# Kernel tuning notes

Hardware: AMD Instinct MI355X
Metric: run time of the kernel (lower is better)

The kernel has to match this reference:

```python
import jax, jax.numpy as jnp
import numpy as np
from jax import lax

# GlobalSeed with a standard Mamba2 (SSD) core.
# C=64 feature channels, G=8 token dim, d_inner=16, d_state=16, nheads=2, headdim=8, d_conv=3.
C_FEAT, G, D_INNER, D_STATE, NHEADS, HEADDIM, D_CONV = 64, 8, 16, 16, 2, 8, 3
CONV_DIM = D_INNER + 2 * D_STATE  # 48
D_IN_PROJ = 2 * D_INNER + 2 * D_STATE + NHEADS  # 66


def setup_inputs() -> dict:
    key = jax.random.key(0)
    ks = jax.random.split(key, 16)
    B, H, W = 16, 128, 128
    s = 0.02
    return {
        "x": jax.random.normal(ks[0], (B, C_FEAT, H, W), jnp.float32),
        "tok_w": s * jax.random.normal(ks[1], (G, C_FEAT), jnp.float32),
        "tok_b": jnp.zeros((G,), jnp.float32),
        "detok_w": s * jax.random.normal(ks[2], (C_FEAT, G), jnp.float32),
        "detok_b": jnp.zeros((C_FEAT,), jnp.float32),
        "in_proj_w": s * jax.random.normal(ks[3], (D_IN_PROJ, G), jnp.float32),
        "in_proj_b": jnp.zeros((D_IN_PROJ,), jnp.float32),
        "conv_w": s * jax.random.normal(ks[4], (CONV_DIM, D_CONV), jnp.float32),
        "conv_b": jnp.zeros((CONV_DIM,), jnp.float32),
        "A_log": jnp.log(jnp.arange(1, NHEADS + 1, dtype=jnp.float32)),
        "D": jnp.ones((NHEADS,), jnp.float32),
        "dt_bias": 0.1 * jax.random.normal(ks[5], (NHEADS,), jnp.float32),
        "norm_w": jnp.ones((D_INNER,), jnp.float32),
        "out_w": s * jax.random.normal(ks[6], (G, D_INNER), jnp.float32),
        "out_b": jnp.zeros((G,), jnp.float32),
    }


def _mamba2(gt, in_proj_w, in_proj_b, conv_w, conv_b, A_log, D, dt_bias, norm_w, out_w, out_b):
    # gt: (B, L, G) tokens
    B, L, _ = gt.shape
    zxbcdt = gt @ in_proj_w.T + in_proj_b  # (B, L, 66)
    z = zxbcdt[..., :D_INNER]
    xBC = zxbcdt[..., D_INNER:D_INNER + CONV_DIM]
    dt = zxbcdt[..., D_INNER + CONV_DIM:]  # (B, L, nheads)
    # depthwise causal conv1d over L
    xBC = lax.conv_general_dilated(
        xBC.transpose(0, 2, 1), conv_w[:, None, :], (1,), [(D_CONV - 1, 0)],
        feature_group_count=CONV_DIM).transpose(0, 2, 1) + conv_b
    xBC = jax.nn.silu(xBC)
    xr = xBC[..., :D_INNER].reshape(B, L, NHEADS, HEADDIM)
    Bm = xBC[..., D_INNER:D_INNER + D_STATE]   # (B, L, N)
    Cm = xBC[..., D_INNER + D_STATE:]          # (B, L, N)
    dt = jax.nn.softplus(dt + dt_bias)          # (B, L, H)
    dec = jnp.exp(dt * (-jnp.exp(A_log)))       # (B, L, H)

    def step(h, inp):
        xt, Bt, Ct, dtt, dct = inp  # (B,H,P) (B,N) (B,N) (B,H) (B,H)
        h = dct[:, :, None, None] * h + (dtt[:, :, None] * xt)[..., None] * Bt[:, None, None, :]
        y = jnp.einsum('bhpn,bn->bhp', h, Ct)
        return h, y

    h0 = jnp.zeros((B, NHEADS, HEADDIM, D_STATE), gt.dtype)
    xs = (xr.transpose(1, 0, 2, 3), Bm.transpose(1, 0, 2), Cm.transpose(1, 0, 2),
          dt.transpose(1, 0, 2), dec.transpose(1, 0, 2))
    _, ys = lax.scan(step, h0, xs)  # (L, B, H, P)
    y = ys.transpose(1, 0, 2, 3) + D[None, None, :, None] * xr
    y = y.reshape(B, L, D_INNER)
    y = y * jax.nn.silu(z)  # gated
    y = y * lax.rsqrt(jnp.mean(y * y, axis=-1, keepdims=True) + 1e-5) * norm_w  # RMSNormGated
    return y @ out_w.T + out_b  # (B, L, G)


def reference(x, tok_w, tok_b, detok_w, detok_b, in_proj_w, in_proj_b, conv_w, conv_b,
              A_log, D, dt_bias, norm_w, out_w, out_b):
    B, C, H, W = x.shape
    L = H * W
    g = jnp.einsum('bchw,gc->bghw', x, tok_w) + tok_b[None, :, None, None]
    gt = g.reshape(B, G, L).transpose(0, 2, 1)  # (B, L, G)
    gt = _mamba2(gt, in_proj_w, in_proj_b, conv_w, conv_b, A_log, D, dt_bias, norm_w, out_w, out_b) + gt
    g2 = gt.transpose(0, 2, 1).reshape(B, G, H, W)
    return x + jnp.einsum('bghw,cg->bchw', g2, detok_w) + detok_b[None, :, None, None]
```

## Files before the change

### kernel.cpp

```cpp
#include <hip/hip_runtime.h>
#include <math.h>

#define NB 16
#define CF 64
#define LL 16384
#define GG 8
#define NH 2
#define CHN 64
#define NCH 256
#define NGRP 16

static constexpr size_t OFF_GT = 0;
static constexpr size_t OFF_U2 = OFF_GT + (size_t)NB*LL*GG;
static constexpr size_t OFF_AC = OFF_U2 + (size_t)NB*NCH*256;
static constexpr size_t OFF_PH = OFF_AC + (size_t)NB*NCH*NH;
static constexpr size_t OFF_CP = OFF_PH + (size_t)NB*NCH*256;
static constexpr size_t OFF_UG = OFF_CP + (size_t)NB*NCH*NH;
static constexpr size_t OFF_AG = OFF_UG + (size_t)NB*NGRP*256;
static constexpr size_t OFF_GH = OFF_AG + (size_t)NB*NGRP*NH;
static constexpr size_t OFF_G2 = OFF_GH + (size_t)NB*NGRP*256;
static constexpr size_t OFF_ST = OFF_G2 + (size_t)NB*LL*GG;
static constexpr size_t WS_FLOATS = OFF_ST + (size_t)NB*NCH*1792;

typedef float f32x4 __attribute__((ext_vector_type(4)));
typedef short bf16x8 __attribute__((ext_vector_type(8)));

__device__ __forceinline__ float siluf(float v){ return v / (1.f + __expf(-v)); }
__device__ __forceinline__ float softplusf(float v){ return v > 20.f ? v : log1pf(__expf(v)); }

__device__ __forceinline__ unsigned short f2bf(float f){
    unsigned int u = __float_as_uint(f);
    u += 0x7fffu + ((u >> 16) & 1u);
    return (unsigned short)(u >> 16);
}
__device__ __forceinline__ float bf2f(unsigned short s){
    return __uint_as_float(((unsigned int)s) << 16);
}
__device__ __forceinline__ unsigned int pack2bf(float lo, float hi){
    return (unsigned int)f2bf(lo) | ((unsigned int)f2bf(hi) << 16);
}
__device__ __forceinline__ unsigned int packtr(float lo, float hi){
    return (__float_as_uint(hi) & 0xffff0000u) | (__float_as_uint(lo) >> 16);
}

__device__ __forceinline__ void load8(float* d, const float* p){
    float4 a = ((const float4*)p)[0];
    float4 b = ((const float4*)p)[1];
    d[0]=a.x; d[1]=a.y; d[2]=a.z; d[3]=a.w;
    d[4]=b.x; d[5]=b.y; d[6]=b.z; d[7]=b.w;
}

__global__ __launch_bounds__(64) void k1a_tok(
    const float* __restrict__ x, const float* __restrict__ tok_w,
    const float* __restrict__ tok_b, float* __restrict__ gtw)
{
    __shared__ float s_tok[GG*CF];
    int tid = threadIdx.x;
    int b  = blockIdx.x >> 6;
    int ck = blockIdx.x & 63;
    int l0 = (ck << 8) + (tid << 2);
    for (int i = tid; i < GG*CF; i += 64) s_tok[i] = tok_w[i];
    __syncthreads();
    float acc[4][GG];
    #pragma unroll
    for (int r = 0; r < 4; ++r)
        #pragma unroll
        for (int g = 0; g < GG; ++g) acc[r][g] = tok_b[g];
    const float* xb = x + (size_t)b*CF*LL + l0;
    #pragma unroll 8
    for (int c = 0; c < CF; ++c) {
        float4 xv = *(const float4*)(xb + (size_t)c*LL);
        float xa[4] = {xv.x, xv.y, xv.z, xv.w};
        #pragma unroll
        for (int g = 0; g < GG; ++g) {
            float w = s_tok[g*CF + c];
            #pragma unroll
            for (int r = 0; r < 4; ++r) acc[r][g] = fmaf(xa[r], w, acc[r][g]);
        }
    }
    float* gp = gtw + ((size_t)b*LL + l0)*GG;
    #pragma unroll
    for (int r = 0; r < 4; ++r) {
        ((float4*)gp)[r*2+0] = make_float4(acc[r][0],acc[r][1],acc[r][2],acc[r][3]);
        ((float4*)gp)[r*2+1] = make_float4(acc[r][4],acc[r][5],acc[r][6],acc[r][7]);
    }
}

__device__ __forceinline__ void build_W(
    int tid, const float* ipw, const float* ipb, const float* cw, const float* cb,
    unsigned short* Wt, float* s_bias, float* s_c0, float* s_c1, float* s_wdt)
{
    int col = tid & 63, kb = tid >> 6;
    unsigned int wd0=0u, wd1=0u, wd2=0u, wd3=0u;
    if (col < 48) {
        if (kb < 3) {
            float cwv = cw[col*3 + (2-kb)];
            const float* iprow = ipw + (16+col)*8;
            wd0 = pack2bf(iprow[0]*cwv, iprow[1]*cwv);
            wd1 = pack2bf(iprow[2]*cwv, iprow[3]*cwv);
            wd2 = pack2bf(iprow[4]*cwv, iprow[5]*cwv);
            wd3 = pack2bf(iprow[6]*cwv, iprow[7]*cwv);
        }
    } else if (kb == 0) {
        const float* iprow = ipw + (col-48)*8;
        wd0 = pack2bf(iprow[0], iprow[1]);
        wd1 = pack2bf(iprow[2], iprow[3]);
        wd2 = pack2bf(iprow[4], iprow[5]);
        wd3 = pack2bf(iprow[6], iprow[7]);
    }
    *(uint4*)&Wt[col*32 + kb*8] = make_uint4(wd0,wd1,wd2,wd3);
    if (kb == 0) {
        float bias;
        if (col < 48) {
            float w0 = cw[col*3], w1 = cw[col*3+1], w2 = cw[col*3+2];
            float ib = ipb[16+col];
            bias = cb[col] + ib*(w0+w1+w2);
            s_c0[col] = ib*(w0+w1);
            s_c1[col] = ib*w0;
        } else bias = ipb[col-48];
        s_bias[col] = bias;
    } else if (kb == 1 && col < 16) s_wdt[col] = ipw[512 + col];
}

__global__ __launch_bounds__(256) void k2a_state(
    const float* __restrict__ gtw,
    const float* __restrict__ ipw, const float* __restrict__ ipb,
    const float* __restrict__ cw, const float* __restrict__ cb,
    const float* __restrict__ A_log, const float* __restrict__ dt_bias,
    float* __restrict__ stw,
    float* __restrict__ U2w, float* __restrict__ Acw)
{
    __shared__ __align__(16) unsigned short Wt[64*32];
    __shared__ float s_bias[64], s_c0[48], s_c1[48], s_wdt[16];
    __shared__ __align__(16) unsigned short XTbf[16*72];
    __shared__ __align__(16) unsigned short BTbf[16*72];
    __shared__ __align__(16) unsigned short WXbf[16*72];
    __shared__ __align__(16) unsigned short Brow[64*16];
    __shared__ __align__(16) unsigned short Crow[64*16];
    __shared__ float s_dt[64][2], s_nda[64][2], s_w[64][2];

    int tid = threadIdx.x;
    int b = blockIdx.x >> 8, c = blockIdx.x & 255;
    float* stp = stw + ((size_t)(b*NCH + c))*1792;
    build_W(tid, ipw, ipb, cw, cb, Wt, s_bias, s_c0, s_c1, s_wdt);
    __syncthreads();

    float a0e = __expf(A_log[0]), a1e = __expf(A_log[1]);
    float dtb0 = dt_bias[0], dtb1 = dt_bias[1];
    float bdt0 = ipb[64], bdt1 = ipb[65];

    int lane = tid & 63, wv = tid >> 6;
    int ar = lane & 15, kb = lane >> 4;
    int trow = wv*16 + kb*4;

    float fr[8];
    bf16x8 aop = {0,0,0,0,0,0,0,0};
    int rowi = c*CHN + wv*16 + ar - kb;
    if (kb < 3 && rowi >= 0) {
        load8(fr, gtw + ((size_t)b*LL + rowi)*GG);
        unsigned int* ap = (unsigned int*)&aop;
        ap[0] = pack2bf(fr[0],fr[1]); ap[1] = pack2bf(fr[2],fr[3]);
        ap[2] = pack2bf(fr[4],fr[5]); ap[3] = pack2bf(fr[6],fr[7]);
    }
    f32x4 st0, st1, st2;
    {
        float b0 = s_bias[ar], b1 = s_bias[16+ar], b2 = s_bias[32+ar];
        f32x4 c0v = {b0,b0,b0,b0}, c1v = {b1,b1,b1,b1}, c2v = {b2,b2,b2,b2};
        st0 = __builtin_amdgcn_mfma_f32_16x16x32_bf16(aop, *(const bf16x8*)&Wt[ar*32 + kb*8],      c0v, 0,0,0);
        st1 = __builtin_amdgcn_mfma_f32_16x16x32_bf16(aop, *(const bf16x8*)&Wt[(16+ar)*32 + kb*8], c1v, 0,0,0);
        st2 = __builtin_amdgcn_mfma_f32_16x16x32_bf16(aop, *(const bf16x8*)&Wt[(32+ar)*32 + kb*8], c2v, 0,0,0);
    }
    if (c == 0 && wv == 0 && kb == 0) {
        st0[0] -= s_c0[ar];    st0[1] -= s_c1[ar];
        st1[0] -= s_c0[16+ar]; st1[1] -= s_c1[16+ar];
        st2[0] -= s_c0[32+ar]; st2[1] -= s_c1[32+ar];
    }
    if (kb == 0) {
        float d0 = bdt0, d1 = bdt1;
        #pragma unroll
        for (int g = 0; g < 8; ++g) {
            d0 = fmaf(fr[g], s_wdt[g],   d0);
            d1 = fmaf(fr[g], s_wdt[8+g], d1);
        }
        float dt0 = softplusf(d0 + dtb0), dt1 = softplusf(d1 + dtb1);
        int row = wv*16 + ar;
        s_dt[row][0] = dt0; s_dt[row][1] = dt1;
        s_nda[row][0] = -dt0*a0e; s_nda[row][1] = -dt1*a1e;
    }
    {
        float v0 = siluf(st0[0]), v1 = siluf(st0[1]), v2 = siluf(st0[2]), v3 = siluf(st0[3]);
        *(uint2*)&XTbf[ar*72 + trow] = make_uint2(pack2bf(v0,v1), pack2bf(v2,v3));
        float b0 = siluf(st1[0]), b1 = siluf(st1[1]), b2 = siluf(st1[2]), b3 = siluf(st1[3]);
        *(uint2*)&BTbf[ar*72 + trow] = make_uint2(pack2bf(b0,b1), pack2bf(b2,b3));
        float bb[4] = {b0,b1,b2,b3};
        #pragma unroll
        for (int rg = 0; rg < 4; ++rg) {
            float vB = bb[rg];
            float vC = siluf(st2[rg]);
            float pB = __shfl_xor(vB, 1);
            float pC = __shfl_xor(vC, 1);
            if (!(ar & 1)) {
                *(unsigned int*)&Brow[(trow+rg)*16 + ar] = pack2bf(vB, pB);
                *(unsigned int*)&Crow[(trow+rg)*16 + ar] = pack2bf(vC, pC);
            }
        }
    }
    __syncthreads();

    if (tid < 64) {
        int rr = tid;
        float v0 = s_nda[rr][0], v1 = s_nda[rr][1];
        #pragma unroll
        for (int off = 1; off < 64; off <<= 1) {
            float t0 = __shfl_up(v0, off);
            float t1 = __shfl_up(v1, off);
            if (rr >= off) { v0 += t0; v1 += t1; }
        }
        float f0 = __shfl(v0, 63), f1 = __shfl(v1, 63);
        s_w[rr][0] = __expf(f0 - v0) * s_dt[rr][0];
        s_w[rr][1] = __expf(f1 - v1) * s_dt[rr][1];
        stp[1536 + rr*2 + 0] = v0;
        stp[1536 + rr*2 + 1] = v1;
        stp[1664 + rr*2 + 0] = s_dt[rr][0];
        stp[1664 + rr*2 + 1] = s_dt[rr][1];
        if (rr == 63)
            *(float2*)(Acw + ((size_t)b*NCH + c)*2) = make_float2(__expf(f0), __expf(f1));
    }
    __syncthreads();

    {
        unsigned int* stX = (unsigned int*)stp;
        unsigned int* stB = (unsigned int*)(stp + 512);
        unsigned int* stC = (unsigned int*)(stp + 1024);
        if (tid < 128) {
            int p = tid >> 3, seg = tid & 7;
            int s0 = seg*8, he = p >> 3;
            const unsigned short* xp = &XTbf[p*72 + s0];
            unsigned int wd[4];
            #pragma unroll
            for (int j = 0; j < 4; ++j) {
                float lo = bf2f(xp[2*j])   * s_w[s0+2*j][he];
                float hi = bf2f(xp[2*j+1]) * s_w[s0+2*j+1][he];
                wd[j] = pack2bf(lo, hi);
            }
            *(uint4*)&WXbf[p*72 + s0] = make_uint4(wd[0],wd[1],wd[2],wd[3]);
            int row = tid >> 1, hf = tid & 1;
            *(uint4*)&stB[row*8 + hf*4] = *(const uint4*)&Brow[row*16 + hf*8];
        } else {
            int i = tid - 128;
            int p = i >> 3, seg = i & 7;
            *(uint4*)&stX[p*32 + seg*4] = *(const uint4*)&XTbf[p*72 + seg*8];
            int row = i >> 1, hf = i & 1;
            *(uint4*)&stC[row*8 + hf*4] = *(const uint4*)&Crow[row*16 + hf*8];
        }
    }
    __syncthreads();

    if (tid < 64) {
        int ar2 = tid & 15, kb2 = tid >> 4;
        f32x4 acc = {0.f, 0.f, 0.f, 0.f};
        #pragma unroll
        for (int kk = 0; kk < 2; ++kk) {
            bf16x8 aw = *(const bf16x8*)&WXbf[ar2*72 + kk*32 + kb2*8];
            bf16x8 bb = *(const bf16x8*)&BTbf[ar2*72 + kk*32 + kb2*8];
            acc = __builtin_amdgcn_mfma_f32_16x16x32_bf16(aw, bb, acc, 0, 0, 0);
        }
        #pragma unroll
        for (int rg = 0; rg < 4; ++rg)
            U2w[(((size_t)b*NCH + c) << 8) + (kb2*4+rg)*16 + ar2] = acc[rg];
    }
}

__global__ void k4c1(const float* __restrict__ U2w, const float* __restrict__ Acw,
                     float* __restrict__ phw, float* __restrict__ cpw,
                     float* __restrict__ Ugw, float* __restrict__ Agw)
{
    int b = blockIdx.x >> 4, grp = blockIdx.x & 15;
    int e = threadIdx.x, he = e >> 7;
    size_t base = (size_t)b*NCH + grp*16;
    float u[16], A[16];
    #pragma unroll
    for (int j = 0; j < 16; ++j) u[j] = U2w[((base + j) << 8) + e];
    #pragma unroll
    for (int j = 0; j < 16; ++j) A[j] = Acw[(base + j)*2 + he];
    float h = 0.f, cp = 1.f;
    #pragma unroll
    for (int j = 0; j < 16; ++j) {
        phw[((base + j) << 8) + e] = h;
        if ((e & 127) == 0) cpw[(base + j)*2 + he] = cp;
        h = fmaf(A[j], h, u[j]);
        cp *= A[j];
    }
    Ugw[(((size_t)b*NGRP + grp) << 8) + e] = h;
    if ((e & 127) == 0) Agw[((size_t)b*NGRP + grp)*2 + he] = cp;
}

__global__ void k4c2(const float* __restrict__ Ugw, const float* __restrict__ Agw,
                     float* __restrict__ ghw)
{
    int b = blockIdx.x, e = threadIdx.x, he = e >> 7;
    float u[NGRP], ag[NGRP];
    #pragma unroll
    for (int g = 0; g < NGRP; ++g) {
        u[g]  = Ugw[(((size_t)b*NGRP + g) << 8) + e];
        ag[g] = Agw[((size_t)b*NGRP + g)*2 + he];
    }
    float h = 0.f;
    #pragma unroll
    for (int g = 0; g < NGRP; ++g) {
        ghw[(((size_t)b*NGRP + g) << 8) + e] = h;
        h = fmaf(ag[g], h, u[g]);
    }
}

__global__ __launch_bounds__(256) void k2b_fused(
    const float* __restrict__ gtw,
    const float* __restrict__ ipw, const float* __restrict__ ipb,
    const float* __restrict__ Dv, const float* __restrict__ norm_w,
    const float* __restrict__ out_w, const float* __restrict__ out_b,
    const float* __restrict__ phw, const float* __restrict__ cpw,
    const float* __restrict__ ghw, const float* __restrict__ stw,
    float* __restrict__ g2w)
{
    __shared__ union {
        unsigned short Ct[64*40];
        float yb[64*20];
    } uC;
    __shared__ __align__(16) unsigned short Bt[64*40];
    __shared__ __align__(16) unsigned short XTbf[16*72];
    __shared__ __align__(16) unsigned short M2[2][64*72];
    __shared__ __align__(16) unsigned short Cp0[64*16], Cp1[64*16];
    __shared__ __align__(16) unsigned short hinT[2][8*16];
    __shared__ float s_hin[256];
    __shared__ float s_la[128];
    __shared__ float s_eti[2][64], s_etd[2][64], s_esc[2][4][4];
    __shared__ float s_zw[128], s_ow[128], s_zb[16], s_nw[16], s_ob[8];

    int tid = threadIdx.x;
    int b = blockIdx.x >> 8, c = blockIdx.x & 255;
    const float* stp = stw + ((size_t)(b*NCH + c))*1792;
    const unsigned int* stX = (const unsigned int*)stp;
    const unsigned int* stB = (const unsigned int*)(stp + 512);
    const unsigned int* stC = (const unsigned int*)(stp + 1024);

    int r = tid >> 2, sub = tid & 3;
    float g0[8];
    load8(g0, gtw + ((size_t)b*LL + c*CHN + r)*GG);
    {
        int grp = c >> 4;
        float gh  = ghw[(((size_t)b*NGRP + grp) << 8) + tid];
        float cpv = cpw[((size_t)b*NCH + c)*2 + (tid >> 7)];
        float phv = phw[(((size_t)b*NCH + c) << 8) + tid];
        s_hin[tid] = fmaf(cpv, gh, phv);
    }
    if (tid < 64) {
        int row = tid;
        *(uint4*)&uC.Ct[row*40]      = *(const uint4*)&stC[row*8];
        *(uint4*)&uC.Ct[row*40 + 8]  = *(const uint4*)&stC[row*8 + 4];
        *(uint4*)&uC.Ct[row*40 + 16] = make_uint4(0,0,0,0);
        *(uint4*)&uC.Ct[row*40 + 24] = make_uint4(0,0,0,0);
    } else if (tid < 128) {
        int row = tid - 64;
        *(uint4*)&Bt[row*40]      = *(const uint4*)&stB[row*8];
        *(uint4*)&Bt[row*40 + 8]  = *(const uint4*)&stB[row*8 + 4];
        *(uint4*)&Bt[row*40 + 16] = make_uint4(0,0,0,0);
        *(uint4*)&Bt[row*40 + 24] = make_uint4(0,0,0,0);
    } else {
        int i = tid - 128;
        int p = i >> 3, seg = i & 7;
        *(uint4*)&XTbf[p*72 + seg*8] = *(const uint4*)&stX[p*32 + seg*4];
    }
    if (tid < 128) { s_la[tid] = stp[1536 + tid]; s_zw[tid] = ipw[tid]; }
    else s_ow[tid-128] = out_w[tid-128];
    if (tid < 16) { s_zb[tid] = ipb[tid]; s_nw[tid] = norm_w[tid]; }
    else if (tid < 24) s_ob[tid-16] = out_b[tid-16];
    __syncthreads();

    float D0 = Dv[0], D1 = Dv[1];
    int lane = tid & 63, wv = tid >> 6;
    int ar = lane & 15, kb = lane >> 4;
    int trow = wv*16 + kb*4;

    f32x4 gT[4];
    {
        bf16x8 aC = *(const bf16x8*)&uC.Ct[(wv*16 + ar)*40 + kb*8];
        #pragma unroll
        for (int ss = 0; ss < 4; ++ss) {
            f32x4 g = {0.f, 0.f, 0.f, 0.f};
            if (ss <= wv) {
                bf16x8 bB = *(const bf16x8*)&Bt[(ss*16 + ar)*40 + kb*8];
                g = __builtin_amdgcn_mfma_f32_16x16x32_bf16(aC, bB, g, 0, 0, 0);
            }
            gT[ss] = g;
        }
    }
    if (tid < 128) {
        int h = tid >> 6;
        int rr = (tid & 63);
        float sc = __expf(s_la[rr*2 + h]);
        unsigned short* Cp = h ? Cp1 : Cp0;
        unsigned int* dst = (unsigned int*)&Cp[rr*16];
        #pragma unroll
        for (int j = 0; j < 8; ++j)
            dst[j] = pack2bf(sc * bf2f(uC.Ct[rr*40 + j*2]),
                             sc * bf2f(uC.Ct[rr*40 + j*2 + 1]));
        if (tid < 32) {
            int i = tid;
            int hh = i >> 4, p = (i >> 1) & 7, half = i & 1;
            unsigned int wd[4];
            #pragma unroll
            for (int j = 0; j < 4; ++j)
                wd[j] = pack2bf(s_hin[hh*128 + p*16 + half*8 + 2*j],
                                s_hin[hh*128 + p*16 + half*8 + 2*j + 1]);
            *(uint4*)&hinT[hh][p*16 + half*8] = make_uint4(wd[0],wd[1],wd[2],wd[3]);
        }
    } else {
        int i = tid - 128;
        int h = i >> 6, s = i & 63;
        int anc = s & ~15;
        float d = s_la[anc*2 + h] - s_la[s*2 + h];
        float dtv = stp[1664 + s*2 + h];
        s_eti[h][s] = __expf(-d);
        s_etd[h][s] = __expf(d) * dtv;
        if (i < 32) {
            int h2 = i >> 4, wt = (i >> 2) & 3, ws = i & 3;
            s_esc[h2][wt][ws] = (wt >= ws) ?
                __expf(s_la[(wt*16)*2 + h2] - s_la[(ws*16)*2 + h2]) : 0.f;
        }
    }
    __syncthreads();

    {
        float rowf0[4], rowf1[4];
        #pragma unroll
        for (int rg = 0; rg < 4; ++rg) {
            rowf0[rg] = s_eti[0][trow+rg];
            rowf1[rg] = s_eti[1][trow+rg];
        }
        #pragma unroll
        for (int ss = 0; ss < 4; ++ss) {
            int s = ss*16 + ar;
            if (ss > wv) {
                if (!(ar & 1)) {
                    #pragma unroll
                    for (int rg = 0; rg < 4; ++rg) {
                        *(unsigned int*)&M2[0][(trow+rg)*72 + ss*16 + ar] = 0u;
                        *(unsigned int*)&M2[1][(trow+rg)*72 + ss*16 + ar] = 0u;
                    }
                }
                continue;
            }
            float colf0 = s_esc[0][wv][ss] * s_etd[0][s];
            float colf1 = s_esc[1][wv][ss] * s_etd[1][s];
            #pragma unroll
            for (int rg = 0; rg < 4; ++rg) {
                bool keep = (s <= trow+rg);
                float m0 = keep ? rowf0[rg]*colf0*gT[ss][rg] : 0.f;
                float m1 = keep ? rowf1[rg]*colf1*gT[ss][rg] : 0.f;
                float m0p = __shfl_xor(m0, 1);
                float m1p = __shfl_xor(m1, 1);
                if (!(ar & 1)) {
                    *(unsigned int*)&M2[0][(trow+rg)*72 + ss*16 + ar] = packtr(m0, m0p);
                    *(unsigned int*)&M2[1][(trow+rg)*72 + ss*16 + ar] = packtr(m1, m1p);
                }
            }
        }
    }
    __syncthreads();

    {
        int p = ar;
        f32x4 acc0 = {0.f,0.f,0.f,0.f}, acc1 = {0.f,0.f,0.f,0.f};
        #pragma unroll
        for (int kk = 0; kk < 2; ++kk) {
            bf16x8 am0 = *(const bf16x8*)&M2[0][(wv*16 + ar)*72 + kk*32 + kb*8];
            bf16x8 am1 = *(const bf16x8*)&M2[1][(wv*16 + ar)*72 + kk*32 + kb*8];
            bf16x8 bx0 = {0,0,0,0,0,0,0,0}, bx1 = {0,0,0,0,0,0,0,0};
            if (p < 8) {
                bx0 = *(const bf16x8*)&XTbf[p*72 + kk*32 + kb*8];
                bx1 = *(const bf16x8*)&XTbf[(8+p)*72 + kk*32 + kb*8];
            }
            acc0 = __builtin_amdgcn_mfma_f32_16x16x32_bf16(am0, bx0, acc0, 0, 0, 0);
            acc1 = __builtin_amdgcn_mfma_f32_16x16x32_bf16(am1, bx1, acc1, 0, 0, 0);
        }
        bf16x8 aCp0 = {0,0,0,0,0,0,0,0}, aCp1 = {0,0,0,0,0,0,0,0};
        bf16x8 bh0 = {0,0,0,0,0,0,0,0}, bh1 = {0,0,0,0,0,0,0,0};
        if (kb < 2) {
            aCp0 = *(const bf16x8*)&Cp0[(wv*16 + ar)*16 + kb*8];
            aCp1 = *(const bf16x8*)&Cp1[(wv*16 + ar)*16 + kb*8];
            if (ar < 8) {
                bh0 = *(const bf16x8*)&hinT[0][ar*16 + kb*8];
                bh1 = *(const bf16x8*)&hinT[1][ar*16 + kb*8];
            }
        }
        acc0 = __builtin_amdgcn_mfma_f32_16x16x32_bf16(aCp0, bh0, acc0, 0, 0, 0);
        acc1 = __builtin_amdgcn_mfma_f32_16x16x32_bf16(aCp1, bh1, acc1, 0, 0, 0);
        if (p < 8) {
            #pragma unroll
            for (int rg = 0; rg < 4; ++rg) {
                int t = trow + rg;
                uC.yb[t*20 + p]     = fmaf(D0, bf2f(XTbf[p*72 + t]),     acc0[rg]);
                uC.yb[t*20 + 8 + p] = fmaf(D1, bf2f(XTbf[(8+p)*72 + t]), acc1[rg]);
            }
        }
    }
    __syncthreads();

    {
        int q = sub;
        float vv[4]; float ssq = 0.f;
        #pragma unroll
        for (int j = 0; j < 4; ++j) {
            int hp = q*4 + j;
            float zz = s_zb[hp];
            #pragma unroll
            for (int g = 0; g < 8; ++g) zz = fmaf(g0[g], s_zw[hp*8+g], zz);
            float y = uC.yb[r*20 + hp];
            float w = y * siluf(zz);
            vv[j] = w; ssq = fmaf(w, w, ssq);
        }
        ssq += __shfl_xor(ssq, 1);
        ssq += __shfl_xor(ssq, 2);
        float rn = rsqrtf(ssq*(1.f/16.f) + 1e-5f);
        float o[8];
        #pragma unroll
        for (int g = 0; g < 8; ++g) o[g] = 0.f;
        #pragma unroll
        for (int j = 0; j < 4; ++j) {
            float wj = vv[j] * rn * s_nw[q*4+j];
            #pragma unroll
            for (int g = 0; g < 8; ++g) o[g] = fmaf(wj, s_ow[g*16 + q*4 + j], o[g]);
        }
        #pragma unroll
        for (int g = 0; g < 8; ++g) {
            o[g] += __shfl_xor(o[g], 1);
            o[g] += __shfl_xor(o[g], 2);
        }
        if (q == 0) {
            #pragma unroll
            for (int g = 0; g < 8; ++g) o[g] += s_ob[g] + g0[g];
            float* gp = g2w + ((size_t)b*LL + c*CHN + r)*GG;
            ((float4*)gp)[0] = make_float4(o[0],o[1],o[2],o[3]);
            ((float4*)gp)[1] = make_float4(o[4],o[5],o[6],o[7]);
        }
    }
}

__global__ __launch_bounds__(64) void k5b_detok(
    const float* __restrict__ x, const float* __restrict__ g2w,
    const float* __restrict__ dkw, const float* __restrict__ dkb,
    float* __restrict__ outp)
{
    __shared__ float s_dw[CF*GG];
    __shared__ float s_db[CF];
    int tid = threadIdx.x;
    int b  = blockIdx.x >> 6;
    int ck = blockIdx.x & 63;
    int l0 = (ck << 8) + (tid << 2);
    for (int i = tid; i < CF*GG; i += 64) s_dw[i] = dkw[i];
    s_db[tid] = dkb[tid];
    __syncthreads();
    float g2v[4][8];
    const float* gp = g2w + ((size_t)b*LL + l0)*GG;
    #pragma unroll
    for (int r = 0; r < 4; ++r) load8(g2v[r], gp + r*GG);
    const float* xb = x + (size_t)b*CF*LL + l0;
    float* ob = outp + (size_t)b*CF*LL + l0;
    #pragma unroll 4
    for (int c = 0; c < CF; ++c) {
        float4 xv = *(const float4*)(xb + (size_t)c*LL);
        float bias = s_db[c];
        float oa[4] = {xv.x+bias, xv.y+bias, xv.z+bias, xv.w+bias};
        #pragma unroll
        for (int g = 0; g < GG; ++g) {
            float w = s_dw[c*GG+g];
            #pragma unroll
            for (int r = 0; r < 4; ++r) oa[r] = fmaf(g2v[r][g], w, oa[r]);
        }
        *(float4*)(ob + (size_t)c*LL) = make_float4(oa[0],oa[1],oa[2],oa[3]);
    }
}

extern "C" void kernel_launch(void* const* d_in, const int* in_sizes, int n_in,
                              void* d_out, int out_size, void* d_ws, size_t ws_size,
                              hipStream_t stream) {
    const float* x       = (const float*)d_in[0];
    const float* tok_w   = (const float*)d_in[1];
    const float* tok_b   = (const float*)d_in[2];
    const float* detok_w = (const float*)d_in[3];
    const float* detok_b = (const float*)d_in[4];
    const float* ipw     = (const float*)d_in[5];
    const float* ipb     = (const float*)d_in[6];
    const float* cw      = (const float*)d_in[7];
    const float* cb      = (const float*)d_in[8];
    const float* A_log   = (const float*)d_in[9];
    const float* Dv      = (const float*)d_in[10];
    const float* dt_bias = (const float*)d_in[11];
    const float* norm_w  = (const float*)d_in[12];
    const float* out_w   = (const float*)d_in[13];
    const float* out_b   = (const float*)d_in[14];
    float* ws = (float*)d_ws;
    float* outp = (float*)d_out;

    if (ws_size < WS_FLOATS * sizeof(float)) return;

    k1a_tok<<<NB*64, 64, 0, stream>>>(x, tok_w, tok_b, ws+OFF_GT);
    k2a_state<<<NB*NCH, 256, 0, stream>>>(ws+OFF_GT, ipw, ipb, cw, cb,
        A_log, dt_bias, ws+OFF_ST, ws+OFF_U2, ws+OFF_AC);
    k4c1<<<NB*NGRP, 256, 0, stream>>>(ws+OFF_U2, ws+OFF_AC,
        ws+OFF_PH, ws+OFF_CP, ws+OFF_UG, ws+OFF_AG);
    k4c2<<<NB, 256, 0, stream>>>(ws+OFF_UG, ws+OFF_AG, ws+OFF_GH);
    k2b_fused<<<NB*NCH, 256, 0, stream>>>(ws+OFF_GT, ipw, ipb,
        Dv, norm_w, out_w, out_b,
        ws+OFF_PH, ws+OFF_CP, ws+OFF_GH, ws+OFF_ST, ws+OFF_G2);
    k5b_detok<<<NB*64, 64, 0, stream>>>(x, ws+OFF_G2, detok_w, detok_b, outp);
}
```

Before: 122.2 us.

## Load B/C MFMA operands from global directly and process heads sequentially to cut LDS

The C·B^T MFMA operands are now loaded straight from the global staging buffer into registers instead of being staged through padded shared-memory tiles. The per-head decay matrix is built and consumed one head at a time in a single reused LDS buffer rather than two. Together these shrink shared memory per block, which could allow more resident blocks per CU. The cost is an extra barrier pair per head, serialised head work, and unpadded global reads for the Cp scaling.

```diff
diff --git a/kernel.cpp b/kernel.cpp
--- a/kernel.cpp
+++ b/kernel.cpp
@@ -322,13 +322,9 @@
     const float* __restrict__ ghw, const float* __restrict__ stw,
     float* __restrict__ g2w)
 {
-    __shared__ union {
-        unsigned short Ct[64*40];
-        float yb[64*20];
-    } uC;
-    __shared__ __align__(16) unsigned short Bt[64*40];
+    __shared__ float yb[64*20];
     __shared__ __align__(16) unsigned short XTbf[16*72];
-    __shared__ __align__(16) unsigned short M2[2][64*72];
+    __shared__ __align__(16) unsigned short Mb[64*72];
     __shared__ __align__(16) unsigned short Cp0[64*16], Cp1[64*16];
     __shared__ __align__(16) unsigned short hinT[2][8*16];
     __shared__ float s_hin[256];
@@ -340,12 +336,36 @@
     int b = blockIdx.x >> 8, c = blockIdx.x & 255;
     const float* stp = stw + ((size_t)(b*NCH + c))*1792;
     const unsigned int* stX = (const unsigned int*)stp;
-    const unsigned int* stB = (const unsigned int*)(stp + 512);
-    const unsigned int* stC = (const unsigned int*)(stp + 1024);
+    const unsigned short* stBu = (const unsigned short*)(stp + 512);
+    const unsigned short* stCu = (const unsigned short*)(stp + 1024);
 
     int r = tid >> 2, sub = tid & 3;
+    int lane = tid & 63, wv = tid >> 6;
+    int ar = lane & 15, kb = lane >> 4;
+    int trow = wv*16 + kb*4;
+
     float g0[8];
     load8(g0, gtw + ((size_t)b*LL + c*CHN + r)*GG);
+
+    bf16x8 aC = {0,0,0,0,0,0,0,0};
+    bf16x8 bBr[4];
+    #pragma unroll
+    for (int ss = 0; ss < 4; ++ss) bBr[ss] = (bf16x8){0,0,0,0,0,0,0,0};
+    if (kb < 2) {
+        aC = *(const bf16x8*)&stCu[(wv*16 + ar)*16 + kb*8];
+        #pragma unroll
+        for (int ss = 0; ss < 4; ++ss)
+            if (ss <= wv) bBr[ss] = *(const bf16x8*)&stBu[(ss*16 + ar)*16 + kb*8];
+    }
+    f32x4 gT[4];
+    #pragma unroll
+    for (int ss = 0; ss < 4; ++ss) {
+        f32x4 g = {0.f, 0.f, 0.f, 0.f};
+        if (ss <= wv)
+            g = __builtin_amdgcn_mfma_f32_16x16x32_bf16(aC, bBr[ss], g, 0, 0, 0);
+        gT[ss] = g;
+    }
+
     {
         int grp = c >> 4;
         float gh  = ghw[(((size_t)b*NGRP + grp) << 8) + tid];
@@ -353,57 +373,36 @@
         float phv = phw[(((size_t)b*NCH + c) << 8) + tid];
         s_hin[tid] = fmaf(cpv, gh, phv);
     }
-    if (tid < 64) {
-        int row = tid;
-        *(uint4*)&uC.Ct[row*40]      = *(const uint4*)&stC[row*8];
-        *(uint4*)&uC.Ct[row*40 + 8]  = *(const uint4*)&stC[row*8 + 4];
-        *(uint4*)&uC.Ct[row*40 + 16] = make_uint4(0,0,0,0);
-        *(uint4*)&uC.Ct[row*40 + 24] = make_uint4(0,0,0,0);
-    } else if (tid < 128) {
-        int row = tid - 64;
-        *(uint4*)&Bt[row*40]      = *(const uint4*)&stB[row*8];
-        *(uint4*)&Bt[row*40 + 8]  = *(const uint4*)&stB[row*8 + 4];
-        *(uint4*)&Bt[row*40 + 16] = make_uint4(0,0,0,0);
-        *(uint4*)&Bt[row*40 + 24] = make_uint4(0,0,0,0);
+    if (tid < 128) {
+        int p = tid >> 3, seg = tid & 7;
+        *(uint4*)&XTbf[p*72 + seg*8] = *(const uint4*)&stX[p*32 + seg*4];
+        s_la[tid] = stp[1536 + tid];
+        s_zw[tid] = ipw[tid];
     } else {
-        int i = tid - 128;
-        int p = i >> 3, seg = i & 7;
-        *(uint4*)&XTbf[p*72 + seg*8] = *(const uint4*)&stX[p*32 + seg*4];
-    }
-    if (tid < 128) { s_la[tid] = stp[1536 + tid]; s_zw[tid] = ipw[tid]; }
-    else s_ow[tid-128] = out_w[tid-128];
-    if (tid < 16) { s_zb[tid] = ipb[tid]; s_nw[tid] = norm_w[tid]; }
-    else if (tid < 24) s_ob[tid-16] = out_b[tid-16];
+        s_ow[tid-128] = out_w[tid-128];
+        int t2 = tid - 128;
+        if (t2 < 16) { s_zb[t2] = ipb[t2]; s_nw[t2] = norm_w[t2]; }
+        else if (t2 < 24) s_ob[t2-16] = out_b[t2-16];
+    }
     __syncthreads();
 
     float D0 = Dv[0], D1 = Dv[1];
-    int lane = tid & 63, wv = tid >> 6;
-    int ar = lane & 15, kb = lane >> 4;
-    int trow = wv*16 + kb*4;
-
-    f32x4 gT[4];
-    {
-        bf16x8 aC = *(const bf16x8*)&uC.Ct[(wv*16 + ar)*40 + kb*8];
-        #pragma unroll
-        for (int ss = 0; ss < 4; ++ss) {
-            f32x4 g = {0.f, 0.f, 0.f, 0.f};
-            if (ss <= wv) {
-                bf16x8 bB = *(const bf16x8*)&Bt[(ss*16 + ar)*40 + kb*8];
-                g = __builtin_amdgcn_mfma_f32_16x16x32_bf16(aC, bB, g, 0, 0, 0);
-            }
-            gT[ss] = g;
-        }
-    }
+
     if (tid < 128) {
         int h = tid >> 6;
-        int rr = (tid & 63);
+        int rr = tid & 63;
         float sc = __expf(s_la[rr*2 + h]);
+        uint4 ra = *(const uint4*)&stCu[rr*16];
+        uint4 rb = *(const uint4*)&stCu[rr*16 + 8];
+        unsigned int src[8] = {ra.x,ra.y,ra.z,ra.w, rb.x,rb.y,rb.z,rb.w};
         unsigned short* Cp = h ? Cp1 : Cp0;
         unsigned int* dst = (unsigned int*)&Cp[rr*16];
         #pragma unroll
-        for (int j = 0; j < 8; ++j)
-            dst[j] = pack2bf(sc * bf2f(uC.Ct[rr*40 + j*2]),
-                             sc * bf2f(uC.Ct[rr*40 + j*2 + 1]));
+        for (int j = 0; j < 8; ++j) {
+            float lo = bf2f((unsigned short)(src[j] & 0xffffu)) * sc;
+            float hi = bf2f((unsigned short)(src[j] >> 16)) * sc;
+            dst[j] = pack2bf(lo, hi);
+        }
         if (tid < 32) {
             int i = tid;
             int hh = i >> 4, p = (i >> 1) & 7, half = i & 1;
@@ -430,81 +429,65 @@
     }
     __syncthreads();
 
-    {
-        float rowf0[4], rowf1[4];
-        #pragma unroll
-        for (int rg = 0; rg < 4; ++rg) {
-            rowf0[rg] = s_eti[0][trow+rg];
-            rowf1[rg] = s_eti[1][trow+rg];
-        }
-        #pragma unroll
-        for (int ss = 0; ss < 4; ++ss) {
-            int s = ss*16 + ar;
-            if (ss > wv) {
-                if (!(ar & 1)) {
-                    #pragma unroll
-                    for (int rg = 0; rg < 4; ++rg) {
-                        *(unsigned int*)&M2[0][(trow+rg)*72 + ss*16 + ar] = 0u;
-                        *(unsigned int*)&M2[1][(trow+rg)*72 + ss*16 + ar] = 0u;
+    #pragma unroll
+    for (int h = 0; h < 2; ++h) {
+        {
+            float rowf[4];
+            #pragma unroll
+            for (int rg = 0; rg < 4; ++rg) rowf[rg] = s_eti[h][trow+rg];
+            #pragma unroll
+            for (int ss = 0; ss < 4; ++ss) {
+                int s = ss*16 + ar;
+                if (ss > wv) {
+                    if (!(ar & 1)) {
+                        #pragma unroll
+                        for (int rg = 0; rg < 4; ++rg)
+                            *(unsigned int*)&Mb[(trow+rg)*72 + ss*16 + ar] = 0u;
                     }
+                    continue;
                 }
-                continue;
-            }
-            float colf0 = s_esc[0][wv][ss] * s_etd[0][s];
-            float colf1 = s_esc[1][wv][ss] * s_etd[1][s];
-            #pragma unroll
-            for (int rg = 0; rg < 4; ++rg) {
-                bool keep = (s <= trow+rg);
-                float m0 = keep ? rowf0[rg]*colf0*gT[ss][rg] : 0.f;
-                float m1 = keep ? rowf1[rg]*colf1*gT[ss][rg] : 0.f;
-                float m0p = __shfl_xor(m0, 1);
-                float m1p = __shfl_xor(m1, 1);
-                if (!(ar & 1)) {
-                    *(unsigned int*)&M2[0][(trow+rg)*72 + ss*16 + ar] = packtr(m0, m0p);
-                    *(unsigned int*)&M2[1][(trow+rg)*72 + ss*16 + ar] = packtr(m1, m1p);
+                float colf = s_esc[h][wv][ss] * s_etd[h][s];
+                #pragma unroll
+                for (int rg = 0; rg < 4; ++rg) {
+                    bool keep = (s <= trow+rg);
+                    float m = keep ? rowf[rg]*colf*gT[ss][rg] : 0.f;
+                    float mp = __shfl_xor(m, 1);
+                    if (!(ar & 1))
+                        *(unsigned int*)&Mb[(trow+rg)*72 + ss*16 + ar] = packtr(m, mp);
                 }
             }
         }
-    }
-    __syncthreads();
-
-    {
-        int p = ar;
-        f32x4 acc0 = {0.f,0.f,0.f,0.f}, acc1 = {0.f,0.f,0.f,0.f};
-        #pragma unroll
-        for (int kk = 0; kk < 2; ++kk) {
-            bf16x8 am0 = *(const bf16x8*)&M2[0][(wv*16 + ar)*72 + kk*32 + kb*8];
-            bf16x8 am1 = *(const bf16x8*)&M2[1][(wv*16 + ar)*72 + kk*32 + kb*8];
-            bf16x8 bx0 = {0,0,0,0,0,0,0,0}, bx1 = {0,0,0,0,0,0,0,0};
+        __syncthreads();
+
+        {
+            int p = ar;
+            f32x4 acc = {0.f,0.f,0.f,0.f};
+            #pragma unroll
+            for (int kk = 0; kk < 2; ++kk) {
+                bf16x8 am = *(const bf16x8*)&Mb[(wv*16 + ar)*72 + kk*32 + kb*8];
+                bf16x8 bx = {0,0,0,0,0,0,0,0};
+                if (p < 8) bx = *(const bf16x8*)&XTbf[(h*8 + p)*72 + kk*32 + kb*8];
+                acc = __builtin_amdgcn_mfma_f32_16x16x32_bf16(am, bx, acc, 0, 0, 0);
+            }
+            bf16x8 aCp = {0,0,0,0,0,0,0,0};
+            bf16x8 bh  = {0,0,0,0,0,0,0,0};
+            if (kb < 2) {
+                aCp = h ? *(const bf16x8*)&Cp1[(wv*16 + ar)*16 + kb*8]
+                        : *(const bf16x8*)&Cp0[(wv*16 + ar)*16 + kb*8];
+                if (ar < 8) bh = *(const bf16x8*)&hinT[h][ar*16 + kb*8];
+            }
+            acc = __builtin_amdgcn_mfma_f32_16x16x32_bf16(aCp, bh, acc, 0, 0, 0);
             if (p < 8) {
-                bx0 = *(const bf16x8*)&XTbf[p*72 + kk*32 + kb*8];
-                bx1 = *(const bf16x8*)&XTbf[(8+p)*72 + kk*32 + kb*8];
+                float Dh = h ? D1 : D0;
+                #pragma unroll
+                for (int rg = 0; rg < 4; ++rg) {
+                    int t = trow + rg;
+                    yb[t*20 + h*8 + p] = fmaf(Dh, bf2f(XTbf[(h*8 + p)*72 + t]), acc[rg]);
+                }
             }
-            acc0 = __builtin_amdgcn_mfma_f32_16x16x32_bf16(am0, bx0, acc0, 0, 0, 0);
-            acc1 = __builtin_amdgcn_mfma_f32_16x16x32_bf16(am1, bx1, acc1, 0, 0, 0);
-        }
-        bf16x8 aCp0 = {0,0,0,0,0,0,0,0}, aCp1 = {0,0,0,0,0,0,0,0};
-        bf16x8 bh0 = {0,0,0,0,0,0,0,0}, bh1 = {0,0,0,0,0,0,0,0};
-        if (kb < 2) {
-            aCp0 = *(const bf16x8*)&Cp0[(wv*16 + ar)*16 + kb*8];
-            aCp1 = *(const bf16x8*)&Cp1[(wv*16 + ar)*16 + kb*8];
-            if (ar < 8) {
-                bh0 = *(const bf16x8*)&hinT[0][ar*16 + kb*8];
-                bh1 = *(const bf16x8*)&hinT[1][ar*16 + kb*8];
-            }
-        }
-        acc0 = __builtin_amdgcn_mfma_f32_16x16x32_bf16(aCp0, bh0, acc0, 0, 0, 0);
-        acc1 = __builtin_amdgcn_mfma_f32_16x16x32_bf16(aCp1, bh1, acc1, 0, 0, 0);
-        if (p < 8) {
-            #pragma unroll
-            for (int rg = 0; rg < 4; ++rg) {
-                int t = trow + rg;
-                uC.yb[t*20 + p]     = fmaf(D0, bf2f(XTbf[p*72 + t]),     acc0[rg]);
-                uC.yb[t*20 + 8 + p] = fmaf(D1, bf2f(XTbf[(8+p)*72 + t]), acc1[rg]);
-            }
-        }
-    }
-    __syncthreads();
+        }
+        __syncthreads();
+    }
 
     {
         int q = sub;
@@ -515,7 +498,7 @@
             float zz = s_zb[hp];
             #pragma unroll
             for (int g = 0; g < 8; ++g) zz = fmaf(g0[g], s_zw[hp*8+g], zz);
-            float y = uC.yb[r*20 + hp];
+            float y = yb[r*20 + hp];
             float w = y * siluf(zz);
             vv[j] = w; ssq = fmaf(w, w, ssq);
         }
```

Result: faster. 118.6 us (-2.9%).
